# Optimization experiments

Measured on AMD Instinct MI355X. Metric: run time of the kernel, lower is better.

The kernel has to match this reference:

```python
import jax, jax.numpy as jnp
import numpy as np


def setup_inputs() -> dict:
    key = jax.random.key(0)
    k1, k2, k3 = jax.random.split(key, 3)
    B, N, D, F = 4, 4096, 128, 128
    features = jax.random.normal(k1, (B, N, D), dtype=jnp.float32)
    A = jax.random.uniform(k2, (B, N, N), dtype=jnp.float32)
    weight = jax.random.normal(k3, (D, F), dtype=jnp.float32) * (6.0 / (D + F)) ** 0.5
    bias = jnp.zeros((F,), dtype=jnp.float32)
    return {"features": features, "A": A, "weight": weight, "bias": bias}


def reference(features, A, weight, bias):
    # aggregate: per-batch adjacency matmul  [B,N,N] @ [B,N,D] -> [B,N,D]
    agg = jnp.einsum("bnm,bmd->bnd", A, features)
    # linear transform + bias + relu  [B,N,D] @ [D,F] -> [B,N,F]
    out = jnp.einsum("bnd,df->bnf", agg, weight) + bias
    return jax.nn.relu(out)
```

## Files before the change

kernel.cpp:

```cpp
#include <hip/hip_runtime.h>
#include <hip/hip_bf16.h>

typedef __attribute__((ext_vector_type(4))) float  float4v;
typedef __attribute__((ext_vector_type(4))) short  short4v;
typedef __attribute__((ext_vector_type(8))) short  short8v;
typedef __attribute__((ext_vector_type(4))) float  f32x4;

__device__ __forceinline__ short f2bf(float f) {
  __hip_bfloat16 h = __float2bfloat16(f);
  return *reinterpret_cast<short*>(&h);
}

__device__ __forceinline__ short8v cvt8(float4v v0, float4v v1) {
  short8v s;
  s[0]=f2bf(v0[0]); s[1]=f2bf(v0[1]); s[2]=f2bf(v0[2]); s[3]=f2bf(v0[3]);
  s[4]=f2bf(v1[0]); s[5]=f2bf(v1[1]); s[6]=f2bf(v1[2]); s[7]=f2bf(v1[3]);
  return s;
}

__device__ __forceinline__ int swz(int row, int k, int ld) {
  return row * ld + (k ^ ((row & 7) << 3));
}

__device__ __forceinline__ void gll16(const void* g, void* l) {
  __builtin_amdgcn_global_load_lds(
      (const __attribute__((address_space(1))) unsigned int*)g,
      (__attribute__((address_space(3))) unsigned int*)l, 16, 0, 0);
}

__global__ __launch_bounds__(256) void k0_wt(const float* __restrict__ W,
                                             short* __restrict__ wt) {
  const int task = blockIdx.x * 256 + threadIdx.x;
  const int f = task & 127;
  const int dc = (task >> 7) * 8;
  short8v s;
#pragma unroll
  for (int j = 0; j < 8; ++j) s[j] = f2bf(W[(size_t)(dc + j) * 128 + f]);
  *(short8v*)(wt + (size_t)f * 128 + dc) = s;
}

__global__ __launch_bounds__(256) void k1_feat_x_w(
    const float* __restrict__ feat, const short* __restrict__ wt,
    short* __restrict__ ht, int N) {
  const int t = threadIdx.x;
  const int batch = blockIdx.y;
  const int m0 = blockIdx.x * 64;
  const int lane = t & 63, wid = t >> 6;
  const int lr = lane & 15, lk = (lane >> 4) * 8;
  const float* pa = feat + (size_t)batch * N * 128
                  + (size_t)(m0 + wid * 16 + lr) * 128 + lk;

  f32x4 acc[8];
#pragma unroll
  for (int j = 0; j < 8; ++j) acc[j] = (f32x4){0.f, 0.f, 0.f, 0.f};

#pragma unroll
  for (int kk = 0; kk < 4; ++kk) {
    float4v v0 = ((const float4v*)(pa + kk * 32))[0];
    float4v v1 = ((const float4v*)(pa + kk * 32))[1];
    short8v a = cvt8(v0, v1);
#pragma unroll
    for (int ni = 0; ni < 8; ++ni) {
      short8v b = *(const short8v*)(wt + (size_t)(ni * 16 + lr) * 128 + kk * 32 + lk);
      acc[ni] = __builtin_amdgcn_mfma_f32_16x16x32_bf16(a, b, acc[ni], 0, 0, 0);
    }
  }

  short* hb = ht + (size_t)batch * 128 * N;
  const int m = m0 + wid * 16 + (lane >> 4) * 4;
#pragma unroll
  for (int ni = 0; ni < 8; ++ni) {
    const int f = ni * 16 + lr;
    short4v s;
#pragma unroll
    for (int r = 0; r < 4; ++r) s[r] = f2bf(acc[ni][r]);
    *(short4v*)(hb + (size_t)f * N + m) = s;
  }
}

__global__ __launch_bounds__(256, 4) void k2_a_x_h(
    const float* __restrict__ A, const short* __restrict__ ht,
    const float* __restrict__ bias, float* __restrict__ out, int N) {
  __shared__ __align__(16) short As[2][16 * 64];
  __shared__ __align__(16) short Hs[2][128 * 64];
  const int t = threadIdx.x;

  const int nwg = gridDim.x * gridDim.y;
  int wg = blockIdx.x + gridDim.x * blockIdx.y;
  wg = (wg & 7) * (nwg >> 3) + (wg >> 3);
  const int mtiles = gridDim.x;
  const int batch = wg / mtiles;
  const int m0 = (wg - batch * mtiles) * 16;

  const float* Ab = A + (size_t)batch * N * N;
  const short* hb = ht + (size_t)batch * 128 * N;

  const int lane = t & 63, wid = t >> 6;
  const int lr = lane & 15, lk = (lane >> 4) * 8;

  const int arow = t >> 4;
  const int akc = (t & 15) * 4;

  const int hf = lane >> 3;
  const int hks = (lane & 7) * 8;

  float4v va;
  auto loadA = [&](int k0) {
    va = *(const float4v*)(Ab + (size_t)(m0 + arow) * N + k0 + akc);
  };
  auto writeA = [&](int buf) {
    short4v s;
#pragma unroll
    for (int i = 0; i < 4; ++i) s[i] = f2bf(va[i]);
    *(short4v*)(&As[buf][swz(arow, akc, 64)]) = s;
  };
  auto stageH = [&](int k0, int buf) {
#pragma unroll
    for (int i = 0; i < 4; ++i) {
      const int fb8 = (wid * 4 + i) * 8;
      const int f = fb8 + hf;
      const short* g = hb + (size_t)f * N + k0 + (hks ^ (hf << 3));
      gll16(g, &Hs[buf][fb8 * 64]);
    }
  };

  f32x4 acc[2];
  acc[0] = (f32x4){0.f, 0.f, 0.f, 0.f};
  acc[1] = (f32x4){0.f, 0.f, 0.f, 0.f};

  loadA(0);
  stageH(0, 0);
  writeA(0);
  __syncthreads();

  const int NT = N / 64;
  for (int tt = 0; tt < NT; ++tt) {
    const int cur = tt & 1;
    const bool pf = (tt + 1 < NT);
    if (pf) {
      loadA((tt + 1) * 64);
      stageH((tt + 1) * 64, cur ^ 1);
    }
#pragma unroll
    for (int kk = 0; kk < 2; ++kk) {
      const int k = kk * 32 + lk;
      short8v a = *(const short8v*)(&As[cur][swz(lr, k, 64)]);
#pragma unroll
      for (int ni = 0; ni < 2; ++ni) {
        short8v b = *(const short8v*)(&Hs[cur][swz(wid * 32 + ni * 16 + lr, k, 64)]);
        acc[ni] = __builtin_amdgcn_mfma_f32_16x16x32_bf16(a, b, acc[ni], 0, 0, 0);
      }
    }
    if (pf) writeA(cur ^ 1);
    __syncthreads();
  }

  float* ob = out + (size_t)batch * N * 128;
#pragma unroll
  for (int ni = 0; ni < 2; ++ni) {
    const int f = wid * 32 + ni * 16 + lr;
    const float bv = bias[f];
    const int mbase = m0 + (lane >> 4) * 4;
#pragma unroll
    for (int r = 0; r < 4; ++r)
      ob[(size_t)(mbase + r) * 128 + f] = fmaxf(acc[ni][r] + bv, 0.f);
  }
}

extern "C" void kernel_launch(void* const* d_in, const int* in_sizes, int n_in,
                              void* d_out, int out_size, void* d_ws, size_t ws_size,
                              hipStream_t stream) {
  const float* feat = (const float*)d_in[0];
  const float* A    = (const float*)d_in[1];
  const float* W    = (const float*)d_in[2];
  const float* bias = (const float*)d_in[3];
  float* out = (float*)d_out;

  const int featN = in_sizes[0];
  const int aN    = in_sizes[1];
  const int BN    = featN / 128;
  const int N     = aN / BN;
  const int Bb    = BN / N;

  short* wt = (short*)d_ws;
  short* ht = wt + 128 * 128;

  dim3 blk(256);
  hipLaunchKernelGGL(k0_wt, dim3(8), blk, 0, stream, W, wt);
  hipLaunchKernelGGL(k1_feat_x_w, dim3(N / 64, Bb), blk, 0, stream, feat, wt, ht, N);
  hipLaunchKernelGGL(k2_a_x_h, dim3(N / 16, Bb), blk, 0, stream, A, ht, bias, out, N);
}
```

Baseline: 93.03 us.

## Stage fp32 A via direct global-to-LDS loads and double the M tile

The main kernel now copies fp32 A tiles straight into shared memory with global_load_lds, using an XOR swizzle, and converts them to bf16 at fragment read time. This replaces the register round-trip through loadA/writeA. The M tile grows from 16 to 32 rows with a 2x2 wave split, so each H tile staged in LDS is reused across twice as many A rows and the grid is halved. The H-producing kernel also transposes its output through shared memory so global stores are coalesced 16-byte writes. In exchange, the A buffers take more LDS because they are held as fp32, which may lower occupancy, and the conversion work moves into the inner loop.

```diff
diff --git a/kernel.cpp b/kernel.cpp
--- a/kernel.cpp
+++ b/kernel.cpp
@@ -42,6 +42,7 @@
 __global__ __launch_bounds__(256) void k1_feat_x_w(
     const float* __restrict__ feat, const short* __restrict__ wt,
     short* __restrict__ ht, int N) {
+  __shared__ short T[128][72];
   const int t = threadIdx.x;
   const int batch = blockIdx.y;
   const int m0 = blockIdx.x * 64;
@@ -66,54 +67,62 @@
     }
   }
 
+  const int mloc = wid * 16 + (lane >> 4) * 4;
+#pragma unroll
+  for (int ni = 0; ni < 8; ++ni) {
+    short4v s;
+#pragma unroll
+    for (int r = 0; r < 4; ++r) s[r] = f2bf(acc[ni][r]);
+    *(short4v*)(&T[ni * 16 + lr][mloc]) = s;
+  }
+  __syncthreads();
+
   short* hb = ht + (size_t)batch * 128 * N;
-  const int m = m0 + wid * 16 + (lane >> 4) * 4;
-#pragma unroll
-  for (int ni = 0; ni < 8; ++ni) {
-    const int f = ni * 16 + lr;
-    short4v s;
-#pragma unroll
-    for (int r = 0; r < 4; ++r) s[r] = f2bf(acc[ni][r]);
-    *(short4v*)(hb + (size_t)f * N + m) = s;
+#pragma unroll
+  for (int it = 0; it < 4; ++it) {
+    const int idx = it * 256 + t;
+    const int f = idx >> 3;
+    const int mc = (idx & 7) * 8;
+    short8v v = *(const short8v*)(&T[f][mc]);
+    *(short8v*)(hb + (size_t)f * N + m0 + mc) = v;
   }
 }
 
 __global__ __launch_bounds__(256, 4) void k2_a_x_h(
     const float* __restrict__ A, const short* __restrict__ ht,
     const float* __restrict__ bias, float* __restrict__ out, int N) {
-  __shared__ __align__(16) short As[2][16 * 64];
+  __shared__ __align__(16) float Asf[2][32 * 64];
   __shared__ __align__(16) short Hs[2][128 * 64];
   const int t = threadIdx.x;
+  const int lane = t & 63, wid = t >> 6;
+  const int mi = wid >> 1, fj = wid & 1;
 
   const int nwg = gridDim.x * gridDim.y;
   int wg = blockIdx.x + gridDim.x * blockIdx.y;
   wg = (wg & 7) * (nwg >> 3) + (wg >> 3);
   const int mtiles = gridDim.x;
   const int batch = wg / mtiles;
-  const int m0 = (wg - batch * mtiles) * 16;
+  const int m0 = (wg - batch * mtiles) * 32;
 
   const float* Ab = A + (size_t)batch * N * N;
   const short* hb = ht + (size_t)batch * 128 * N;
 
-  const int lane = t & 63, wid = t >> 6;
   const int lr = lane & 15, lk = (lane >> 4) * 8;
 
-  const int arow = t >> 4;
-  const int akc = (t & 15) * 4;
-
+  const int ar = lane >> 4;
+  const int ac = (lane & 15) * 4;
+  auto stageA = [&](int k0, int buf) {
+#pragma unroll
+    for (int i = 0; i < 2; ++i) {
+      const int r4 = wid * 8 + i * 4;
+      const int row = r4 + ar;
+      const float* g = Ab + (size_t)(m0 + row) * N + k0
+                     + (ac ^ ((row & 7) << 2));
+      gll16(g, &Asf[buf][r4 * 64]);
+    }
+  };
   const int hf = lane >> 3;
   const int hks = (lane & 7) * 8;
-
-  float4v va;
-  auto loadA = [&](int k0) {
-    va = *(const float4v*)(Ab + (size_t)(m0 + arow) * N + k0 + akc);
-  };
-  auto writeA = [&](int buf) {
-    short4v s;
-#pragma unroll
-    for (int i = 0; i < 4; ++i) s[i] = f2bf(va[i]);
-    *(short4v*)(&As[buf][swz(arow, akc, 64)]) = s;
-  };
   auto stageH = [&](int k0, int buf) {
 #pragma unroll
     for (int i = 0; i < 4; ++i) {
@@ -124,43 +133,48 @@
     }
   };
 
-  f32x4 acc[2];
-  acc[0] = (f32x4){0.f, 0.f, 0.f, 0.f};
-  acc[1] = (f32x4){0.f, 0.f, 0.f, 0.f};
-
-  loadA(0);
+  auto rdA = [&](int buf, int r, int c0) -> float4v {
+    const char* base = (const char*)&Asf[buf][0];
+    return *(const float4v*)(base + r * 256 + ((c0 * 4) ^ ((r & 7) << 4)));
+  };
+
+  f32x4 acc[4];
+#pragma unroll
+  for (int j = 0; j < 4; ++j) acc[j] = (f32x4){0.f, 0.f, 0.f, 0.f};
+
+  stageA(0, 0);
   stageH(0, 0);
-  writeA(0);
   __syncthreads();
 
   const int NT = N / 64;
+  const int arow = mi * 16 + lr;
   for (int tt = 0; tt < NT; ++tt) {
     const int cur = tt & 1;
-    const bool pf = (tt + 1 < NT);
-    if (pf) {
-      loadA((tt + 1) * 64);
+    if (tt + 1 < NT) {
+      stageA((tt + 1) * 64, cur ^ 1);
       stageH((tt + 1) * 64, cur ^ 1);
     }
 #pragma unroll
     for (int kk = 0; kk < 2; ++kk) {
       const int k = kk * 32 + lk;
-      short8v a = *(const short8v*)(&As[cur][swz(lr, k, 64)]);
-#pragma unroll
-      for (int ni = 0; ni < 2; ++ni) {
-        short8v b = *(const short8v*)(&Hs[cur][swz(wid * 32 + ni * 16 + lr, k, 64)]);
+      float4v a0 = rdA(cur, arow, k);
+      float4v a1 = rdA(cur, arow, k + 4);
+      short8v a = cvt8(a0, a1);
+#pragma unroll
+      for (int ni = 0; ni < 4; ++ni) {
+        short8v b = *(const short8v*)(&Hs[cur][swz(fj * 64 + ni * 16 + lr, k, 64)]);
         acc[ni] = __builtin_amdgcn_mfma_f32_16x16x32_bf16(a, b, acc[ni], 0, 0, 0);
       }
     }
-    if (pf) writeA(cur ^ 1);
     __syncthreads();
   }
 
   float* ob = out + (size_t)batch * N * 128;
 #pragma unroll
-  for (int ni = 0; ni < 2; ++ni) {
-    const int f = wid * 32 + ni * 16 + lr;
+  for (int ni = 0; ni < 4; ++ni) {
+    const int f = fj * 64 + ni * 16 + lr;
     const float bv = bias[f];
-    const int mbase = m0 + (lane >> 4) * 4;
+    const int mbase = m0 + mi * 16 + (lane >> 4) * 4;
 #pragma unroll
     for (int r = 0; r < 4; ++r)
       ob[(size_t)(mbase + r) * 128 + f] = fmaxf(acc[ni][r] + bv, 0.f);
@@ -185,8 +199,7 @@
   short* wt = (short*)d_ws;
   short* ht = wt + 128 * 128;
 
-  dim3 blk(256);
-  hipLaunchKernelGGL(k0_wt, dim3(8), blk, 0, stream, W, wt);
-  hipLaunchKernelGGL(k1_feat_x_w, dim3(N / 64, Bb), blk, 0, stream, feat, wt, ht, N);
-  hipLaunchKernelGGL(k2_a_x_h, dim3(N / 16, Bb), blk, 0, stream, A, ht, bias, out, N);
-}
+  hipLaunchKernelGGL(k0_wt, dim3(8), dim3(256), 0, stream, W, wt);
+  hipLaunchKernelGGL(k1_feat_x_w, dim3(N / 64, Bb), dim3(256), 0, stream, feat, wt, ht, N);
+  hipLaunchKernelGGL(k2_a_x_h, dim3(N / 32, Bb), dim3(256), 0, stream, A, ht, bias, out, N);
+}
```

Measured after the change: 89.74 us. -3.5%, faster.
